# Kernel optimization log

Measured on AMD Instinct MI355X. Metric: run time of the kernel, lower is better.

## Reference

```python
import jax, jax.numpy as jnp
import numpy as np

B, S, D, H, HD = 2, 4096, 1024, 16, 64   # batch, seq, hidden, heads, head_dim
BLOCK, W = 64, 8                          # block size, local window in blocks (512 tokens)
ROPE_BASE = 10000.0


def _rope_tables(seq_len, dim, dtype):
    inv_freq = 1.0 / (ROPE_BASE ** (jnp.arange(0, dim, 2, dtype=jnp.float32) / dim))
    t = jnp.arange(seq_len, dtype=jnp.float32)
    freqs = jnp.einsum('i,j->ij', t, inv_freq)          # [S, dim/2]
    emb = jnp.concatenate([freqs, freqs], axis=-1)       # [S, dim]
    return jnp.cos(emb).astype(dtype), jnp.sin(emb).astype(dtype)


def _rotate_half(x):
    x1, x2 = x[..., : x.shape[-1] // 2], x[..., x.shape[-1] // 2:]
    return jnp.concatenate([-x2, x1], axis=-1)


def _apply_rope(q, k, position_ids):
    # q, k: [B, H, S, HD]; position_ids: [B, S]
    cos_t, sin_t = _rope_tables(S, HD, q.dtype)
    cos = cos_t[position_ids][:, None, :, :]             # [B, 1, S, HD]
    sin = sin_t[position_ids][:, None, :, :]
    q_emb = q * cos + _rotate_half(q) * sin
    k_emb = k * cos + _rotate_half(k) * sin
    return q_emb, k_emb


def _block_sparse_attention(q, k, v):
    # Causal block-sparse (sliding window of W blocks), DeepSpeed-style layout.
    # q, k, v: [B, H, S, HD]
    nb = S // BLOCK
    scale = 1.0 / jnp.sqrt(jnp.asarray(HD, q.dtype))
    qb = q.reshape(B, H, nb, BLOCK, HD)
    kb = k.reshape(B, H, nb, BLOCK, HD)
    vb = v.reshape(B, H, nb, BLOCK, HD)
    # block-column indices attended by each block-row: i-W+1 .. i
    idx = jnp.arange(nb)[:, None] - jnp.arange(W - 1, -1, -1)[None, :]   # [nb, W]
    valid = idx >= 0
    idxc = jnp.clip(idx, 0, nb - 1)
    kg = kb[:, :, idxc]                                   # [B, H, nb, W, BLOCK, HD]
    vg = vb[:, :, idxc]
    scores = jnp.einsum('bhnqd,bhnwkd->bhnqwk', qb, kg) * scale  # [B,H,nb,BLOCK,W,BLOCK]
    # absolute positions for causal mask within the window
    qpos = (jnp.arange(nb) * BLOCK)[:, None, None, None] + jnp.arange(BLOCK)[None, :, None, None]  # [nb,BLOCK,1,1]
    kpos = (idxc * BLOCK)[:, None, :, None] + jnp.arange(BLOCK)[None, None, None, :]               # [nb,1,W,BLOCK]
    mask = (kpos <= qpos) & valid[:, None, :, None]       # [nb, BLOCK, W, BLOCK]
    neg = jnp.asarray(-1e9, scores.dtype)
    scores = jnp.where(mask[None, None], scores, neg)
    scores = scores.reshape(B, H, nb, BLOCK, W * BLOCK)
    probs = jax.nn.softmax(scores, axis=-1)
    out = jnp.einsum('bhnqk,bhnkd->bhnqd', probs, vg.reshape(B, H, nb, W * BLOCK, HD))
    return out.reshape(B, H, S, HD)


def setup_inputs() -> dict:
    key = jax.random.key(0)
    ks = jax.random.split(key, 5)
    hidden_states = jax.random.normal(ks[0], (B, S, D), dtype=jnp.float32)
    position_ids = jnp.tile(jnp.arange(S, dtype=jnp.int32)[None, :], (B, 1))
    w_init = lambda k: (jax.random.normal(k, (D, D), dtype=jnp.float32) * 0.02)
    return {
        'hidden_states': hidden_states,
        'position_ids': position_ids,
        'wq': w_init(ks[1]),  # stored [in, out]
        'wk': w_init(ks[2]),
        'wv': w_init(ks[3]),
        'wo': w_init(ks[4]),
    }


def reference(hidden_states, position_ids, wq, wk, wv, wo):
    q = jnp.einsum('bsd,de->bse', hidden_states, wq).reshape(B, S, H, HD).transpose(0, 2, 1, 3)
    k = jnp.einsum('bsd,de->bse', hidden_states, wk).reshape(B, S, H, HD).transpose(0, 2, 1, 3)
    v = jnp.einsum('bsd,de->bse', hidden_states, wv).reshape(B, S, H, HD).transpose(0, 2, 1, 3)
    q, k = _apply_rope(q, k, position_ids)
    attn = _block_sparse_attention(q, k, v)               # [B, H, S, HD]
    attn = attn.transpose(0, 2, 1, 3).reshape(B, S, D)
    return jnp.einsum('bsd,de->bse', attn, wo)
```

## Files before the change

kernel.cpp:

```cpp
#include <hip/hip_runtime.h>
#include <cstdint>
#include <cstddef>

#define B_ 2
#define S_ 4096
#define D_ 1024
#define H_ 16
#define HD_ 64
#define NB_ 64
#define W_ 8
#define M_ (B_*S_)

#define QSCALE 0.18033688011112042f
#define LOG2_10000_OVER_32 0.41524101186092034f

typedef __bf16 bf16_t;
typedef __bf16 bf16x8 __attribute__((ext_vector_type(8)));
typedef float f32x4 __attribute__((ext_vector_type(4)));

#define GLOAD_LDS16(gp, lp) \
  __builtin_amdgcn_global_load_lds((__attribute__((address_space(1))) void*)(gp), \
                                   (__attribute__((address_space(3))) void*)(lp), 16, 0, 0)

__global__ void cast_bf16_kernel(const float* __restrict__ x, bf16_t* __restrict__ y, int n4) {
  int i = blockIdx.x * 256 + threadIdx.x;
  if (i >= n4) return;
  float4 v = ((const float4*)x)[i];
  union { bf16_t b[4]; uint2 u; } cv;
  cv.b[0] = (bf16_t)v.x; cv.b[1] = (bf16_t)v.y; cv.b[2] = (bf16_t)v.z; cv.b[3] = (bf16_t)v.w;
  ((uint2*)y)[i] = cv.u;
}

__global__ void transpose_cast_kernel(const float* __restrict__ w0, const float* __restrict__ w1,
                                      const float* __restrict__ w2, const float* __restrict__ w3,
                                      bf16_t* __restrict__ out) {
  const float* w = (blockIdx.z == 0) ? w0 : (blockIdx.z == 1) ? w1 : (blockIdx.z == 2) ? w2 : w3;
  bf16_t* wt = out + (size_t)blockIdx.z * D_ * D_;
  __shared__ float tile[32][33];
  int x = blockIdx.x * 32 + threadIdx.x;
  int y0 = blockIdx.y * 32;
  for (int i = threadIdx.y; i < 32; i += 8)
    tile[i][threadIdx.x] = w[(size_t)(y0 + i) * D_ + x];
  __syncthreads();
  int x2 = blockIdx.y * 32 + threadIdx.x;
  int y2 = blockIdx.x * 32;
  for (int i = threadIdx.y; i < 32; i += 8)
    wt[(size_t)(y2 + i) * D_ + x2] = (bf16_t)tile[threadIdx.x][i];
}

template<bool OBF>
__global__ __launch_bounds__(256) void gemm128(const bf16_t* __restrict__ A,
                                               const bf16_t* __restrict__ BtBase,
                                               void* __restrict__ Cbase,
                                               bf16_t* __restrict__ vt_out,
                                               const int* __restrict__ pos_ids) {
  const bf16_t* Bt = BtBase + (size_t)blockIdx.z * D_ * D_;
  const int mb = blockIdx.y * 128, nb = blockIdx.x * 128;
  const int tid = threadIdx.x;
  const int wid = tid >> 6, lane = tid & 63;
  const int quad = lane >> 4, l16 = lane & 15;
  const int wr = wid >> 1, wc = wid & 1;

  __shared__ bf16_t As[128 * 32];
  __shared__ bf16_t Bs[128 * 32];

  f32x4 acc[4][4];
#pragma unroll
  for (int mi = 0; mi < 4; ++mi)
#pragma unroll
    for (int ni = 0; ni < 4; ++ni)
      acc[mi][ni] = (f32x4){0.f, 0.f, 0.f, 0.f};

  const int acol = (lane & 3) * 8;
  const int arow0 = wid * 32 + (lane >> 2);
  const bf16_t* gA = A + (size_t)(mb + arow0) * D_ + acol;
  const bf16_t* gB = Bt + (size_t)(nb + arow0) * D_ + acol;

  for (int kt = 0; kt < 32; ++kt) {
    const int k0 = kt * 32;
    __syncthreads();
#pragma unroll
    for (int c = 0; c < 2; ++c) {
      GLOAD_LDS16(gA + (size_t)c * 16 * D_ + k0, As + (wid * 2 + c) * 512);
      GLOAD_LDS16(gB + (size_t)c * 16 * D_ + k0, Bs + (wid * 2 + c) * 512);
    }
    __syncthreads();
    bf16x8 af[4], bfr[4];
#pragma unroll
    for (int mi = 0; mi < 4; ++mi)
      af[mi] = *(const bf16x8*)&As[(wr * 64 + mi * 16 + l16) * 32 + quad * 8];
#pragma unroll
    for (int ni = 0; ni < 4; ++ni)
      bfr[ni] = *(const bf16x8*)&Bs[(wc * 64 + ni * 16 + l16) * 32 + quad * 8];
#pragma unroll
    for (int mi = 0; mi < 4; ++mi)
#pragma unroll
      for (int ni = 0; ni < 4; ++ni)
        acc[mi][ni] = __builtin_amdgcn_mfma_f32_16x16x32_bf16(af[mi], bfr[ni], acc[mi][ni], 0, 0, 0);
  }

  if constexpr (OBF) {
    if (blockIdx.z < 2) {
      bf16_t* Cp = (bf16_t*)Cbase + (size_t)blockIdx.z * M_ * D_;
      const float qsc = (blockIdx.z == 0) ? QSCALE : 1.0f;
      float invf[2];
#pragma unroll
      for (int ni = 0; ni < 2; ++ni)
        invf[ni] = __builtin_exp2f(-(float)(ni * 16 + l16) * LOG2_10000_OVER_32);
#pragma unroll
      for (int mi = 0; mi < 4; ++mi)
#pragma unroll
        for (int r = 0; r < 4; ++r) {
          int row = mb + wr * 64 + mi * 16 + quad * 4 + r;
          float fpos = (float)pos_ids[row];
#pragma unroll
          for (int ni = 0; ni < 2; ++ni) {
            float sn, cs;
            __sincosf(fpos * invf[ni], &sn, &cs);
            float x1 = acc[mi][ni][r], x2 = acc[mi][ni + 2][r];
            int col = nb + wc * 64 + ni * 16 + l16;
            Cp[(size_t)row * D_ + col]      = (bf16_t)((x1 * cs - x2 * sn) * qsc);
            Cp[(size_t)row * D_ + col + 32] = (bf16_t)((x2 * cs + x1 * sn) * qsc);
          }
        }
    } else {
      int g = 2 * blockIdx.y + wr;
      int bb = g >> 6, sblk = g & 63;
      int hh = 2 * blockIdx.x + wc;
      size_t vbase = (size_t)(bb * H_ + hh) * HD_ * S_;
#pragma unroll
      for (int ni = 0; ni < 4; ++ni) {
        int d = ni * 16 + l16;
        union { bf16_t bv[16]; uint4 u[2]; } pk;
#pragma unroll
        for (int r = 0; r < 4; ++r)
#pragma unroll
          for (int mi = 0; mi < 4; ++mi)
            pk.bv[r * 4 + mi] = (bf16_t)acc[mi][ni][r];
        size_t addr = vbase + (size_t)d * S_ + sblk * 64 + quad * 16;
        *(uint4*)&vt_out[addr]     = pk.u[0];
        *(uint4*)&vt_out[addr + 8] = pk.u[1];
      }
    }
  } else {
    float* Cp = (float*)Cbase;
#pragma unroll
    for (int mi = 0; mi < 4; ++mi)
#pragma unroll
      for (int ni = 0; ni < 4; ++ni)
#pragma unroll
        for (int r = 0; r < 4; ++r) {
          int row = mb + wr * 64 + mi * 16 + quad * 4 + r;
          int col = nb + wc * 64 + ni * 16 + l16;
          Cp[(size_t)row * D_ + col] = acc[mi][ni][r];
        }
  }
}

__global__ __launch_bounds__(256) void attn_kernel(const bf16_t* __restrict__ q,
                                                   const bf16_t* __restrict__ k,
                                                   const bf16_t* __restrict__ vt,
                                                   bf16_t* __restrict__ o) {
  const int m = blockIdx.x, h = blockIdx.y, b = blockIdx.z;
  const int n0 = m * 2, n1 = n0 + 1;
  const int tid = threadIdx.x;
  const int wid = tid >> 6, lane = tid & 63;
  const int quad = lane >> 4, l16 = lane & 15;

  __shared__ bf16_t Ks[64 * 72];
  __shared__ bf16_t Vs[64 * 72];
  __shared__ bf16_t Ps[4][16 * 72];

  const size_t hoff = (size_t)h * HD_;
  const size_t vtbase = (size_t)(b * H_ + h) * HD_ * S_;
  const size_t rowb[2] = {(size_t)(b * S_ + n0 * 64), (size_t)(b * S_ + n1 * 64)};

  bf16x8 aq[2][2];
#pragma unroll
  for (int x = 0; x < 2; ++x) {
    const bf16_t* qr = q + (rowb[x] + wid * 16 + l16) * D_ + hoff;
    aq[x][0] = *(const bf16x8*)(qr + quad * 8);
    aq[x][1] = *(const bf16x8*)(qr + 32 + quad * 8);
  }

  f32x4 o_acc[2][4];
  float lsum[2][4];
#pragma unroll
  for (int x = 0; x < 2; ++x)
#pragma unroll
    for (int t = 0; t < 4; ++t) {
      o_acc[x][t] = (f32x4){0.f, 0.f, 0.f, 0.f};
      lsum[x][t] = 0.f;
    }

  const int srow = tid >> 3;
  const int scol = (tid & 7) * 8;

  const int kb0 = (n0 >= W_ - 1) ? n0 - (W_ - 1) : 0;
  for (int kb = kb0; kb <= n1; ++kb) {
    __syncthreads();
    const size_t krow = (size_t)(b * S_ + kb * 64);
#pragma unroll
    for (int it = 0; it < 2; ++it) {
      int r = it * 32 + srow;
      *(uint4*)&Ks[r * 72 + scol] = *(const uint4*)&k[(krow + r) * D_ + hoff + scol];
      *(uint4*)&Vs[r * 72 + scol] = *(const uint4*)&vt[vtbase + (size_t)r * S_ + kb * 64 + scol];
    }
    __syncthreads();

#pragma unroll
    for (int x = 0; x < 2; ++x) {
      const int nx = n0 + x;
      if (x == 0 ? (kb > n0) : (kb < n1 - (W_ - 1))) continue;

      f32x4 sacc[4];
#pragma unroll
      for (int t = 0; t < 4; ++t) sacc[t] = (f32x4){0.f, 0.f, 0.f, 0.f};
#pragma unroll
      for (int t = 0; t < 4; ++t) {
        bf16x8 bk0 = *(const bf16x8*)&Ks[(t * 16 + l16) * 72 + quad * 8];
        bf16x8 bk1 = *(const bf16x8*)&Ks[(t * 16 + l16) * 72 + 32 + quad * 8];
        sacc[t] = __builtin_amdgcn_mfma_f32_16x16x32_bf16(aq[x][0], bk0, sacc[t], 0, 0, 0);
        sacc[t] = __builtin_amdgcn_mfma_f32_16x16x32_bf16(aq[x][1], bk1, sacc[t], 0, 0, 0);
      }

      const bool diag = (kb == nx);
#pragma unroll
      for (int r = 0; r < 4; ++r) {
        int qpos = wid * 16 + quad * 4 + r;
        union { bf16_t bv[4]; uint2 u; } pk;
        float rs = 0.f;
#pragma unroll
        for (int t = 0; t < 4; ++t) {
          float p = __builtin_exp2f(sacc[t][r]);
          if (diag && (t * 16 + l16 > qpos)) p = 0.f;
          rs += p;
          pk.bv[t] = (bf16_t)p;
        }
        lsum[x][r] += rs;
        *(uint2*)&Ps[wid][(quad * 4 + r) * 72 + l16 * 4] = pk.u;
      }

      bf16x8 pa0 = *(const bf16x8*)&Ps[wid][l16 * 72 + quad * 8];
      bf16x8 pa1 = *(const bf16x8*)&Ps[wid][l16 * 72 + 32 + quad * 8];
#pragma unroll
      for (int t = 0; t < 4; ++t) {
        bf16x8 vb0 = *(const bf16x8*)&Vs[(t * 16 + l16) * 72 + quad * 8];
        bf16x8 vb1 = *(const bf16x8*)&Vs[(t * 16 + l16) * 72 + 32 + quad * 8];
        o_acc[x][t] = __builtin_amdgcn_mfma_f32_16x16x32_bf16(pa0, vb0, o_acc[x][t], 0, 0, 0);
        o_acc[x][t] = __builtin_amdgcn_mfma_f32_16x16x32_bf16(pa1, vb1, o_acc[x][t], 0, 0, 0);
      }
    }
  }

#pragma unroll
  for (int x = 0; x < 2; ++x) {
    float inv[4];
#pragma unroll
    for (int r = 0; r < 4; ++r) {
      float s = lsum[x][r];
#pragma unroll
      for (int off = 1; off < 16; off <<= 1) s += __shfl_xor(s, off);
      inv[r] = 1.f / s;
    }
#pragma unroll
    for (int t = 0; t < 4; ++t)
#pragma unroll
      for (int r = 0; r < 4; ++r) {
        int row = wid * 16 + quad * 4 + r;
        int col = t * 16 + l16;
        o[(rowb[x] + row) * D_ + hoff + col] = (bf16_t)(o_acc[x][t][r] * inv[r]);
      }
  }
}

extern "C" void kernel_launch(void* const* d_in, const int* in_sizes, int n_in,
                              void* d_out, int out_size, void* d_ws, size_t ws_size,
                              hipStream_t stream) {
  const float* hs = (const float*)d_in[0];
  const int* pos  = (const int*)d_in[1];
  const float* wq = (const float*)d_in[2];
  const float* wk = (const float*)d_in[3];
  const float* wv = (const float*)d_in[4];
  const float* wo = (const float*)d_in[5];

  bf16_t* ws   = (bf16_t*)d_ws;
  bf16_t* hsb  = ws;
  bf16_t* wT   = hsb + (size_t)M_ * D_;
  bf16_t* qkv  = wT + (size_t)4 * D_ * D_;
  bf16_t* attn = qkv + (size_t)3 * M_ * D_;
  bf16_t* qw  = qkv;
  bf16_t* kw  = qkv + (size_t)M_ * D_;
  bf16_t* vtg = qkv + (size_t)2 * M_ * D_;

  cast_bf16_kernel<<<(M_ * D_ / 4 + 255) / 256, 256, 0, stream>>>(hs, hsb, M_ * D_ / 4);
  transpose_cast_kernel<<<dim3(D_ / 32, D_ / 32, 4), dim3(32, 8), 0, stream>>>(wq, wk, wv, wo, wT);
  gemm128<true><<<dim3(D_ / 128, M_ / 128, 3), 256, 0, stream>>>(hsb, wT, (void*)qkv, vtg, pos);
  attn_kernel<<<dim3(NB_ / 2, H_, B_), 256, 0, stream>>>(qw, kw, vtg, attn);
  gemm128<false><<<dim3(D_ / 128, M_ / 128, 1), 256, 0, stream>>>(attn, wT + (size_t)3 * D_ * D_, d_out, nullptr, pos);
}
```

Measured before the change: 245.6 us.

## Replace QKV GEMM with 256x256-tile, 4-stage pipelined kernel using 512 threads

```diff
diff --git a/kernel.cpp b/kernel.cpp
--- a/kernel.cpp
+++ b/kernel.cpp
@@ -48,6 +48,139 @@
     wt[(size_t)(y2 + i) * D_ + x2] = (bf16_t)tile[threadIdx.x][i];
 }
 
+__global__ __launch_bounds__(512, 2) void gemm_qkv256(const bf16_t* __restrict__ A,
+                                                      const bf16_t* __restrict__ Bt,
+                                                      bf16_t* __restrict__ qkv,
+                                                      bf16_t* __restrict__ vt_out,
+                                                      const int* __restrict__ pos_ids) {
+  const int bid = blockIdx.x;
+  const int sid = (bid & 7) * 48 + (bid >> 3);
+  const int mb = sid / 12, nb = sid % 12;
+  const int mbase = mb * 256, nbase = nb * 256;
+  const int tid = threadIdx.x;
+  const int wid = tid >> 6, lane = tid & 63;
+  const int quad = lane >> 4, l16 = lane & 15;
+  const int wr = wid >> 2, wc = wid & 3;
+
+  __shared__ bf16_t lds[4 * 16384];
+
+  const int srow = wid * 16 + (lane >> 2);
+  const int scol = (lane & 3) * 8;
+  const bf16_t* gAb = A  + (size_t)(mbase + srow) * D_ + scol;
+  const bf16_t* gBb = Bt + (size_t)(nbase + srow) * D_ + scol;
+
+#define LDSA(b) (lds + (b) * 16384)
+#define LDSB(b) (lds + (b) * 16384 + 8192)
+#define STAGE_A(kt) do { bf16_t* p_ = LDSA((kt) & 3) + wid * 512; \
+    GLOAD_LDS16(gAb + (kt) * 32, p_); \
+    GLOAD_LDS16(gAb + (size_t)128 * D_ + (kt) * 32, p_ + 4096); } while (0)
+#define STAGE_B(kt) do { bf16_t* p_ = LDSB((kt) & 3) + wid * 512; \
+    GLOAD_LDS16(gBb + (kt) * 32, p_); \
+    GLOAD_LDS16(gBb + (size_t)128 * D_ + (kt) * 32, p_ + 4096); } while (0)
+#define WAITV(n) asm volatile("s_waitcnt vmcnt(" #n ")" ::: "memory")
+#define BAR() do { __builtin_amdgcn_s_barrier(); asm volatile("" ::: "memory"); } while (0)
+
+  f32x4 acc[8][4];
+#pragma unroll
+  for (int m = 0; m < 8; ++m)
+#pragma unroll
+    for (int n = 0; n < 4; ++n) acc[m][n] = (f32x4){0.f, 0.f, 0.f, 0.f};
+
+#define PHASE(kt, mh, STG, WT) do { \
+    const bf16_t* Ab_ = LDSA((kt) & 3); \
+    const bf16_t* Bb_ = LDSB((kt) & 3); \
+    bf16x8 af_[4], bf_[4]; \
+    _Pragma("unroll") \
+    for (int m = 0; m < 4; ++m) \
+      af_[m] = *(const bf16x8*)&Ab_[(wr * 128 + (mh) * 64 + m * 16 + l16) * 32 + quad * 8]; \
+    _Pragma("unroll") \
+    for (int n = 0; n < 4; ++n) \
+      bf_[n] = *(const bf16x8*)&Bb_[(wc * 64 + n * 16 + l16) * 32 + quad * 8]; \
+    STG; WT; \
+    BAR(); \
+    __builtin_amdgcn_s_setprio(1); \
+    _Pragma("unroll") \
+    for (int m = 0; m < 4; ++m) \
+      _Pragma("unroll") \
+      for (int n = 0; n < 4; ++n) \
+        acc[(mh) * 4 + m][n] = \
+            __builtin_amdgcn_mfma_f32_16x16x32_bf16(af_[m], bf_[n], acc[(mh) * 4 + m][n], 0, 0, 0); \
+    __builtin_amdgcn_s_setprio(0); \
+    BAR(); \
+  } while (0)
+
+  STAGE_A(0); STAGE_B(0); STAGE_A(1); STAGE_B(1); STAGE_A(2); STAGE_B(2);
+  WAITV(8);
+  BAR();
+
+  for (int kt = 0; kt < 29; ++kt) {
+    PHASE(kt, 0, STAGE_A(kt + 3), (void)0);
+    PHASE(kt, 1, STAGE_B(kt + 3), WAITV(8));
+  }
+  PHASE(29, 0, (void)0, (void)0);
+  PHASE(29, 1, (void)0, WAITV(4));
+  PHASE(30, 0, (void)0, (void)0);
+  PHASE(30, 1, (void)0, WAITV(0));
+  PHASE(31, 0, (void)0, (void)0);
+  PHASE(31, 1, (void)0, (void)0);
+
+  const int zsl = nb >> 2;
+  if (zsl < 2) {
+    bf16_t* Cp = qkv + (size_t)zsl * M_ * D_;
+    const float qsc = (zsl == 0) ? QSCALE : 1.0f;
+    float invf[2];
+#pragma unroll
+    for (int ni = 0; ni < 2; ++ni)
+      invf[ni] = __builtin_exp2f(-(float)(ni * 16 + l16) * LOG2_10000_OVER_32);
+    const int colb = (nb & 3) * 256 + wc * 64;
+#pragma unroll
+    for (int m = 0; m < 8; ++m) {
+#pragma unroll
+      for (int r = 0; r < 4; ++r) {
+        int row = mbase + wr * 128 + m * 16 + quad * 4 + r;
+        float fpos = (float)pos_ids[row];
+#pragma unroll
+        for (int ni = 0; ni < 2; ++ni) {
+          float sn, cs;
+          __sincosf(fpos * invf[ni], &sn, &cs);
+          float x1 = acc[m][ni][r], x2 = acc[m][ni + 2][r];
+          int col = colb + ni * 16 + l16;
+          Cp[(size_t)row * D_ + col]      = (bf16_t)((x1 * cs - x2 * sn) * qsc);
+          Cp[(size_t)row * D_ + col + 32] = (bf16_t)((x2 * cs + x1 * sn) * qsc);
+        }
+      }
+    }
+  } else {
+    const int h = (nb & 3) * 4 + wc;
+#pragma unroll
+    for (int mh = 0; mh < 2; ++mh) {
+      int rowblk = mb * 4 + wr * 2 + mh;
+      int bb = rowblk >> 6, sblk = rowblk & 63;
+      size_t vbase = (size_t)(bb * H_ + h) * HD_ * S_;
+#pragma unroll
+      for (int n = 0; n < 4; ++n) {
+        int d = n * 16 + l16;
+        union { bf16_t bv[16]; uint4 u[2]; } pk;
+#pragma unroll
+        for (int r = 0; r < 4; ++r)
+#pragma unroll
+          for (int mi = 0; mi < 4; ++mi)
+            pk.bv[r * 4 + mi] = (bf16_t)acc[mh * 4 + mi][n][r];
+        size_t addr = vbase + (size_t)d * S_ + (size_t)sblk * 64 + quad * 16;
+        *(uint4*)&vt_out[addr]     = pk.u[0];
+        *(uint4*)&vt_out[addr + 8] = pk.u[1];
+      }
+    }
+  }
+#undef PHASE
+#undef STAGE_A
+#undef STAGE_B
+#undef LDSA
+#undef LDSB
+#undef WAITV
+#undef BAR
+}
+
 template<bool OBF>
 __global__ __launch_bounds__(256) void gemm128(const bf16_t* __restrict__ A,
                                                const bf16_t* __restrict__ BtBase,
@@ -100,48 +233,6 @@
   }
 
   if constexpr (OBF) {
-    if (blockIdx.z < 2) {
-      bf16_t* Cp = (bf16_t*)Cbase + (size_t)blockIdx.z * M_ * D_;
-      const float qsc = (blockIdx.z == 0) ? QSCALE : 1.0f;
-      float invf[2];
-#pragma unroll
-      for (int ni = 0; ni < 2; ++ni)
-        invf[ni] = __builtin_exp2f(-(float)(ni * 16 + l16) * LOG2_10000_OVER_32);
-#pragma unroll
-      for (int mi = 0; mi < 4; ++mi)
-#pragma unroll
-        for (int r = 0; r < 4; ++r) {
-          int row = mb + wr * 64 + mi * 16 + quad * 4 + r;
-          float fpos = (float)pos_ids[row];
-#pragma unroll
-          for (int ni = 0; ni < 2; ++ni) {
-            float sn, cs;
-            __sincosf(fpos * invf[ni], &sn, &cs);
-            float x1 = acc[mi][ni][r], x2 = acc[mi][ni + 2][r];
-            int col = nb + wc * 64 + ni * 16 + l16;
-            Cp[(size_t)row * D_ + col]      = (bf16_t)((x1 * cs - x2 * sn) * qsc);
-            Cp[(size_t)row * D_ + col + 32] = (bf16_t)((x2 * cs + x1 * sn) * qsc);
-          }
-        }
-    } else {
-      int g = 2 * blockIdx.y + wr;
-      int bb = g >> 6, sblk = g & 63;
-      int hh = 2 * blockIdx.x + wc;
-      size_t vbase = (size_t)(bb * H_ + hh) * HD_ * S_;
-#pragma unroll
-      for (int ni = 0; ni < 4; ++ni) {
-        int d = ni * 16 + l16;
-        union { bf16_t bv[16]; uint4 u[2]; } pk;
-#pragma unroll
-        for (int r = 0; r < 4; ++r)
-#pragma unroll
-          for (int mi = 0; mi < 4; ++mi)
-            pk.bv[r * 4 + mi] = (bf16_t)acc[mi][ni][r];
-        size_t addr = vbase + (size_t)d * S_ + sblk * 64 + quad * 16;
-        *(uint4*)&vt_out[addr]     = pk.u[0];
-        *(uint4*)&vt_out[addr + 8] = pk.u[1];
-      }
-    }
   } else {
     float* Cp = (float*)Cbase;
 #pragma unroll
@@ -295,7 +386,7 @@
 
   cast_bf16_kernel<<<(M_ * D_ / 4 + 255) / 256, 256, 0, stream>>>(hs, hsb, M_ * D_ / 4);
   transpose_cast_kernel<<<dim3(D_ / 32, D_ / 32, 4), dim3(32, 8), 0, stream>>>(wq, wk, wv, wo, wT);
-  gemm128<true><<<dim3(D_ / 128, M_ / 128, 3), 256, 0, stream>>>(hsb, wT, (void*)qkv, vtg, pos);
+  gemm_qkv256<<<dim3(384), dim3(512), 0, stream>>>(hsb, wT, qkv, vtg, pos);
   attn_kernel<<<dim3(NB_ / 2, H_, B_), 256, 0, stream>>>(qw, kw, vtg, attn);
   gemm128<false><<<dim3(D_ / 128, M_ / 128, 1), 256, 0, stream>>>(attn, wT + (size_t)3 * D_ * D_, d_out, nullptr, pos);
 }
```

Result: slower. 253.2 us (+3.1%).
